# Kernel optimization log

Measured on AMD Instinct MI355X. Metric: run time of the kernel, lower is better.

Reference implementation:

```python
import jax, jax.numpy as jnp
import numpy as np

B, N, DIN = 8, 50000, 16
E, M, CH = 800000, 25000, 64
C_HALF = CH // 2


def setup_inputs() -> dict:
    key = jax.random.key(0)
    ks = jax.random.split(key, 9)
    x = jax.random.normal(ks[0], (B, N, DIN), dtype=jnp.float32)
    adj_rows = jax.random.randint(ks[1], (E,), 0, N, dtype=jnp.int32)
    adj_cols = jax.random.randint(ks[2], (E,), 0, N, dtype=jnp.int32)
    adj_vals = jax.random.uniform(ks[3], (E,), dtype=jnp.float32)
    centroids = jax.random.randint(ks[4], (M,), 0, N, dtype=jnp.int32)
    # Conv1d(kernel_size=1) weights == dense [out, in] matrices
    W_lin = jax.random.normal(ks[5], (C_HALF, DIN), dtype=jnp.float32) * (1.0 / np.sqrt(DIN))
    b_lin = jax.random.normal(ks[6], (C_HALF,), dtype=jnp.float32) * 0.01
    W_eye = jax.random.normal(ks[7], (C_HALF, DIN), dtype=jnp.float32) * (1.0 / np.sqrt(DIN))
    b_eye = jax.random.normal(ks[8], (C_HALF,), dtype=jnp.float32) * 0.01
    return {"x": x, "adj_rows": adj_rows, "adj_cols": adj_cols, "adj_vals": adj_vals,
            "centroids": centroids, "W_lin": W_lin, "b_lin": b_lin,
            "W_eye": W_eye, "b_eye": b_eye}


def reference(x, adj_rows, adj_cols, adj_vals, centroids, W_lin, b_lin, W_eye, b_eye):
    # x: [B, N, DIN] -> permute to channels-first [B, DIN, N]
    xc = jnp.transpose(x, (0, 2, 1))
    # eye branch: 1x1 conv == pointwise linear over channel dim
    eye_x = jnp.einsum('bcn,oc->bon', xc, W_eye) + b_eye[None, :, None]  # [B, C/2, N]
    # SpMM aggregation: adj @ x.T where x is [B*DIN, N]
    xt = xc.reshape(-1, xc.shape[-1]).T                      # [N, B*DIN]
    msgs = adj_vals[:, None] * xt[adj_cols]                  # [E, B*DIN] gather
    agg = jax.ops.segment_sum(msgs, adj_rows, num_segments=xt.shape[0])  # [N, B*DIN] scatter-add
    xa = agg.T.reshape(xc.shape)                             # [B, DIN, N]
    lin_x = jnp.einsum('bcn,oc->bon', xa, W_lin) + b_lin[None, :, None]  # [B, C/2, N]
    out = jax.nn.relu(jnp.concatenate([lin_x, eye_x], axis=1))  # [B, C, N]
    out = out[:, :, centroids]                               # gather centroid nodes [B, C, M]
    return jnp.transpose(out, (0, 2, 1))                     # [B, M, C]
```

## Files before the change

kernel.cpp:

```cpp
#include <hip/hip_runtime.h>

#define DIN   16
#define BB    8
#define FDIM  128
#define CHALF 32
#define CH    64
#define CAP   52
#define CAP2  16

__device__ __forceinline__ unsigned bf16rne(float f) {
    unsigned u = __float_as_uint(f);
    return (u + 0x7FFFu + ((u >> 16) & 1u)) >> 16;
}

__global__ __launch_bounds__(256) void prep_kernel(
    const float4* __restrict__ x4, uint2* __restrict__ xt2, int N,
    const int* __restrict__ centroids, int* __restrict__ seen,
    int* __restrict__ rankid, int* __restrict__ active_list,
    int* __restrict__ nactive, int* __restrict__ cnt2, int* __restrict__ mlist,
    int M) {
    int y = blockIdx.y;
    int t = blockIdx.x * 256 + threadIdx.x;
    if (y < BB) {
        if (t >= N * 4) return;
        int n = t >> 2;
        int q = t & 3;
        float4 v = x4[(long long)y * N * 4 + t];
        uint2 o;
        o.x = bf16rne(v.x) | (bf16rne(v.y) << 16);
        o.y = bf16rne(v.z) | (bf16rne(v.w) << 16);
        xt2[(long long)n * 32 + y * 4 + q] = o;
    } else {
        if (t >= M) return;
        int n = centroids[t];
        if (atomicExch(&seen[n], 1) == 0) {
            int r = atomicAdd(nactive, 1);
            rankid[n] = r + 1;
            active_list[r] = n;
        }
        int pos = atomicAdd(&cnt2[n], 1);
        if (pos < CAP2) mlist[n * CAP2 + pos] = t;
    }
}

__global__ __launch_bounds__(256) void bin_kernel(
    const int* __restrict__ rows, const int* __restrict__ cols,
    const float* __restrict__ vals, const int* __restrict__ rankid,
    int* __restrict__ cnt, int2* __restrict__ bins, int E) {
    int idx = blockIdx.x * blockDim.x + threadIdx.x;
    int e0 = idx * 2;
    if (e0 >= E) return;
    int2   r2 = ((const int2*)rows)[idx];
    int2   c2 = ((const int2*)cols)[idx];
    float2 v2 = ((const float2*)vals)[idx];
    int rr0 = rankid[r2.x];
    if (rr0 != 0) {
        int a = rr0 - 1;
        int pos = atomicAdd(&cnt[a], 1);
        if (pos < CAP)
            bins[(long long)a * CAP + pos] = make_int2(c2.x, __float_as_int(v2.x));
    }
    if (e0 + 1 < E) {
        int rr1 = rankid[r2.y];
        if (rr1 != 0) {
            int a = rr1 - 1;
            int pos = atomicAdd(&cnt[a], 1);
            if (pos < CAP)
                bins[(long long)a * CAP + pos] = make_int2(c2.y, __float_as_int(v2.y));
        }
    }
}

__global__ __launch_bounds__(256) void gather_kernel(
    const uint2* __restrict__ xt2, const int* __restrict__ cnt,
    const int2* __restrict__ bins, const int* __restrict__ active_list,
    const int* __restrict__ nactive,
    const int* __restrict__ cnt2, const int* __restrict__ mlist,
    const float* __restrict__ W_lin, const float* __restrict__ b_lin,
    const float* __restrict__ W_eye, const float* __restrict__ b_eye,
    float* __restrict__ out, int M) {
    int tid = threadIdx.x;
    int w = tid >> 6;
    int l = tid & 63;

    __shared__ float sWc[DIN][CH + 1];
    __shared__ float sb[CH];
    __shared__ float sagg[4][FDIM];
    __shared__ float sx[4][FDIM];

    #pragma unroll
    for (int i = tid; i < CH * DIN; i += 256) {
        int o = i >> 4, cc = i & 15;
        sWc[cc][o] = (o < CHALF) ? W_lin[i] : W_eye[i - CHALF * DIN];
    }
    if (tid < CHALF) sb[tid] = b_lin[tid];
    else if (tid < CH) sb[tid] = b_eye[tid - CHALF];
    __syncthreads();

    int a = blockIdx.x * 4 + w;
    if (a >= *nactive) return;
    int n = active_list[a];
    int c = min(cnt[a], CAP);

    int g = l >> 5;
    int s = l & 31;

    int2 myedge = make_int2(0, 0);
    if (l < c) myedge = bins[(long long)a * CAP + l];
    uint2 xraw = make_uint2(0u, 0u);
    if (g == 0) xraw = xt2[(long long)n * 32 + s];

    int iters = (c + 3) >> 2;
    float4 acc = make_float4(0.f, 0.f, 0.f, 0.f);
    for (int i = 0; i < iters; ++i) {
        int k0 = 4 * i + g;
        int k1 = k0 + 2;
        int   col0 = __shfl(myedge.x, k0);
        float v0   = __int_as_float(__shfl(myedge.y, k0));
        int   col1 = __shfl(myedge.x, k1);
        float v1   = __int_as_float(__shfl(myedge.y, k1));
        uint2 u0 = xt2[(long long)col0 * 32 + s];
        uint2 u1 = xt2[(long long)col1 * 32 + s];
        acc.x += v0 * __uint_as_float(u0.x << 16);
        acc.y += v0 * __uint_as_float(u0.x & 0xFFFF0000u);
        acc.z += v0 * __uint_as_float(u0.y << 16);
        acc.w += v0 * __uint_as_float(u0.y & 0xFFFF0000u);
        acc.x += v1 * __uint_as_float(u1.x << 16);
        acc.y += v1 * __uint_as_float(u1.x & 0xFFFF0000u);
        acc.z += v1 * __uint_as_float(u1.y << 16);
        acc.w += v1 * __uint_as_float(u1.y & 0xFFFF0000u);
    }
    acc.x += __shfl_xor(acc.x, 32);
    acc.y += __shfl_xor(acc.y, 32);
    acc.z += __shfl_xor(acc.z, 32);
    acc.w += __shfl_xor(acc.w, 32);
    if (g == 0) {
        ((float4*)sagg[w])[s] = acc;
        float4 xr;
        xr.x = __uint_as_float(xraw.x << 16);
        xr.y = __uint_as_float(xraw.x & 0xFFFF0000u);
        xr.z = __uint_as_float(xraw.y << 16);
        xr.w = __uint_as_float(xraw.y & 0xFFFF0000u);
        ((float4*)sx[w])[s] = xr;
    }

    int o = l;
    float wreg[DIN];
    #pragma unroll
    for (int cc = 0; cc < DIN; ++cc) wreg[cc] = sWc[cc][o];
    const float* src = (o < CHALF) ? sagg[w] : sx[w];
    float bias = sb[o];
    float res[BB];
    #pragma unroll
    for (int b = 0; b < BB; ++b) {
        float r = bias;
        #pragma unroll
        for (int cc = 0; cc < DIN; ++cc) r += wreg[cc] * src[b * DIN + cc];
        res[b] = fmaxf(r, 0.f);
    }

    int nm = min(cnt2[n], CAP2);
    for (int mm = 0; mm < nm; ++mm) {
        int m = mlist[n * CAP2 + mm];
        float* dst = out + (long long)m * CH + o;
        #pragma unroll
        for (int b = 0; b < BB; ++b)
            dst[(long long)b * M * CH] = res[b];
    }
}

extern "C" void kernel_launch(void* const* d_in, const int* in_sizes, int n_in,
                              void* d_out, int out_size, void* d_ws, size_t ws_size,
                              hipStream_t stream) {
    const float* x        = (const float*)d_in[0];
    const int*   adj_rows = (const int*)d_in[1];
    const int*   adj_cols = (const int*)d_in[2];
    const float* adj_vals = (const float*)d_in[3];
    const int*   cents    = (const int*)d_in[4];
    const float* W_lin    = (const float*)d_in[5];
    const float* b_lin    = (const float*)d_in[6];
    const float* W_eye    = (const float*)d_in[7];
    const float* b_eye    = (const float*)d_in[8];
    float* out = (float*)d_out;

    const int E = in_sizes[1];
    const int M = in_sizes[4];
    const int N = in_sizes[0] / (BB * DIN);

    char* p = (char*)d_ws;
    uint2* xt2   = (uint2*)p;   p += (size_t)N * 32 * sizeof(uint2);
    int2*  bins  = (int2*)p;    p += (size_t)M * CAP * sizeof(int2);
    int*   mlist = (int*)p;     p += (size_t)N * CAP2 * sizeof(int);
    int*   alist = (int*)p;     p += (size_t)M * sizeof(int);
    char* zbase = p;
    int* seen    = (int*)p;     p += (size_t)N * sizeof(int);
    int* rankid  = (int*)p;     p += (size_t)N * sizeof(int);
    int* cnt     = (int*)p;     p += (size_t)M * sizeof(int);
    int* cnt2    = (int*)p;     p += (size_t)N * sizeof(int);
    int* nactive = (int*)p;     p += 16 * sizeof(int);
    size_t zbytes = (size_t)(p - zbase);

    hipMemsetAsync(zbase, 0, zbytes, stream);

    dim3 pgrid((N * 4 + 255) / 256, BB + 1);
    prep_kernel<<<pgrid, 256, 0, stream>>>((const float4*)x, xt2, N,
                                           cents, seen, rankid, alist, nactive,
                                           cnt2, mlist, M);

    bin_kernel<<<(E / 2 + 255) / 256, 256, 0, stream>>>(adj_rows, adj_cols, adj_vals,
                                                        rankid, cnt, bins, E);

    int gblocks = (M + 3) / 4;
    gather_kernel<<<gblocks, 256, 0, stream>>>(xt2, cnt, bins, alist, nactive,
                                               cnt2, mlist,
                                               W_lin, b_lin, W_eye, b_eye, out, M);
}
```

Before: 159.4 us.

## Fuse memset, prep, bin and gather into one cooperative persistent kernel

Replaces the memset and three separate kernel launches with a single cooperative kernel. A bounded grid of persistent blocks uses grid-stride loops and separates the zeroing, transpose/centroid-marking, edge binning and gather/linear phases with grid.sync(). The intent is to remove launch overheads and inter-kernel gaps. In exchange, every phase is limited to the capped grid, which trims parallelism in the gather phase, and each grid-wide barrier has its own cost.

```diff
diff --git a/kernel.cpp b/kernel.cpp
--- a/kernel.cpp
+++ b/kernel.cpp
@@ -1,4 +1,7 @@
 #include <hip/hip_runtime.h>
+#include <hip/hip_cooperative_groups.h>
+
+namespace cg = cooperative_groups;
 
 #define DIN   16
 #define BB    8
@@ -7,31 +10,57 @@
 #define CH    64
 #define CAP   52
 #define CAP2  16
+#define NCU   256
 
 __device__ __forceinline__ unsigned bf16rne(float f) {
     unsigned u = __float_as_uint(f);
     return (u + 0x7FFFu + ((u >> 16) & 1u)) >> 16;
 }
 
-__global__ __launch_bounds__(256) void prep_kernel(
+__global__ __launch_bounds__(256, 4) void fused_kernel(
     const float4* __restrict__ x4, uint2* __restrict__ xt2, int N,
-    const int* __restrict__ centroids, int* __restrict__ seen,
-    int* __restrict__ rankid, int* __restrict__ active_list,
-    int* __restrict__ nactive, int* __restrict__ cnt2, int* __restrict__ mlist,
-    int M) {
-    int y = blockIdx.y;
-    int t = blockIdx.x * 256 + threadIdx.x;
-    if (y < BB) {
-        if (t >= N * 4) return;
-        int n = t >> 2;
-        int q = t & 3;
-        float4 v = x4[(long long)y * N * 4 + t];
+    const int* __restrict__ centroids, int* __restrict__ zbase, int zwords,
+    int* __restrict__ seen, int* __restrict__ rankid,
+    int* __restrict__ active_list, int* __restrict__ nactive,
+    int* __restrict__ cnt2, int* __restrict__ mlist, int M,
+    const int* __restrict__ rows, const int* __restrict__ cols,
+    const float* __restrict__ vals, int* __restrict__ cnt,
+    int2* __restrict__ bins, int E,
+    const float* __restrict__ W_lin, const float* __restrict__ b_lin,
+    const float* __restrict__ W_eye, const float* __restrict__ b_eye,
+    float* __restrict__ out)
+{
+    cg::grid_group grid = cg::this_grid();
+    const int tid   = threadIdx.x;
+    const int gtid  = blockIdx.x * 256 + tid;
+    const int gsize = gridDim.x * 256;
+
+    __shared__ float sWc[DIN][CH + 1];
+    __shared__ float sb[CH];
+    __shared__ float sagg[4][FDIM];
+    __shared__ float sx[4][FDIM];
+
+    for (int i = tid; i < CH * DIN; i += 256) {
+        int o = i >> 4, cc = i & 15;
+        sWc[cc][o] = (o < CHALF) ? W_lin[i] : W_eye[i - CHALF * DIN];
+    }
+    if (tid < CHALF) sb[tid] = b_lin[tid];
+    else if (tid < CH) sb[tid] = b_eye[tid - CHALF];
+
+    for (int i = gtid; i < zwords; i += gsize) zbase[i] = 0;
+
+    grid.sync();
+
+    const int TW = N * 32;
+    for (int i = gtid; i < TW; i += gsize) {
+        int n = i >> 5, slot = i & 31, b = slot >> 2, q = slot & 3;
+        float4 v = x4[((long long)b * N + n) * 4 + q];
         uint2 o;
         o.x = bf16rne(v.x) | (bf16rne(v.y) << 16);
         o.y = bf16rne(v.z) | (bf16rne(v.w) << 16);
-        xt2[(long long)n * 32 + y * 4 + q] = o;
-    } else {
-        if (t >= M) return;
+        xt2[i] = o;
+    }
+    for (int t = gtid; t < M; t += gsize) {
         int n = centroids[t];
         if (atomicExch(&seen[n], 1) == 0) {
             int r = atomicAdd(nactive, 1);
@@ -41,26 +70,21 @@
         int pos = atomicAdd(&cnt2[n], 1);
         if (pos < CAP2) mlist[n * CAP2 + pos] = t;
     }
-}
-
-__global__ __launch_bounds__(256) void bin_kernel(
-    const int* __restrict__ rows, const int* __restrict__ cols,
-    const float* __restrict__ vals, const int* __restrict__ rankid,
-    int* __restrict__ cnt, int2* __restrict__ bins, int E) {
-    int idx = blockIdx.x * blockDim.x + threadIdx.x;
-    int e0 = idx * 2;
-    if (e0 >= E) return;
-    int2   r2 = ((const int2*)rows)[idx];
-    int2   c2 = ((const int2*)cols)[idx];
-    float2 v2 = ((const float2*)vals)[idx];
-    int rr0 = rankid[r2.x];
-    if (rr0 != 0) {
-        int a = rr0 - 1;
-        int pos = atomicAdd(&cnt[a], 1);
-        if (pos < CAP)
-            bins[(long long)a * CAP + pos] = make_int2(c2.x, __float_as_int(v2.x));
-    }
-    if (e0 + 1 < E) {
+
+    grid.sync();
+
+    const int EP = E >> 1;
+    for (int idx = gtid; idx < EP; idx += gsize) {
+        int2   r2 = ((const int2*)rows)[idx];
+        int2   c2 = ((const int2*)cols)[idx];
+        float2 v2 = ((const float2*)vals)[idx];
+        int rr0 = rankid[r2.x];
+        if (rr0 != 0) {
+            int a = rr0 - 1;
+            int pos = atomicAdd(&cnt[a], 1);
+            if (pos < CAP)
+                bins[(long long)a * CAP + pos] = make_int2(c2.x, __float_as_int(v2.x));
+        }
         int rr1 = rankid[r2.y];
         if (rr1 != 0) {
             int a = rr1 - 1;
@@ -69,110 +93,90 @@
                 bins[(long long)a * CAP + pos] = make_int2(c2.y, __float_as_int(v2.y));
         }
     }
-}
-
-__global__ __launch_bounds__(256) void gather_kernel(
-    const uint2* __restrict__ xt2, const int* __restrict__ cnt,
-    const int2* __restrict__ bins, const int* __restrict__ active_list,
-    const int* __restrict__ nactive,
-    const int* __restrict__ cnt2, const int* __restrict__ mlist,
-    const float* __restrict__ W_lin, const float* __restrict__ b_lin,
-    const float* __restrict__ W_eye, const float* __restrict__ b_eye,
-    float* __restrict__ out, int M) {
-    int tid = threadIdx.x;
-    int w = tid >> 6;
-    int l = tid & 63;
-
-    __shared__ float sWc[DIN][CH + 1];
-    __shared__ float sb[CH];
-    __shared__ float sagg[4][FDIM];
-    __shared__ float sx[4][FDIM];
-
-    #pragma unroll
-    for (int i = tid; i < CH * DIN; i += 256) {
-        int o = i >> 4, cc = i & 15;
-        sWc[cc][o] = (o < CHALF) ? W_lin[i] : W_eye[i - CHALF * DIN];
-    }
-    if (tid < CHALF) sb[tid] = b_lin[tid];
-    else if (tid < CH) sb[tid] = b_eye[tid - CHALF];
-    __syncthreads();
-
-    int a = blockIdx.x * 4 + w;
-    if (a >= *nactive) return;
-    int n = active_list[a];
-    int c = min(cnt[a], CAP);
-
-    int g = l >> 5;
-    int s = l & 31;
-
-    int2 myedge = make_int2(0, 0);
-    if (l < c) myedge = bins[(long long)a * CAP + l];
-    uint2 xraw = make_uint2(0u, 0u);
-    if (g == 0) xraw = xt2[(long long)n * 32 + s];
-
-    int iters = (c + 3) >> 2;
-    float4 acc = make_float4(0.f, 0.f, 0.f, 0.f);
-    for (int i = 0; i < iters; ++i) {
-        int k0 = 4 * i + g;
-        int k1 = k0 + 2;
-        int   col0 = __shfl(myedge.x, k0);
-        float v0   = __int_as_float(__shfl(myedge.y, k0));
-        int   col1 = __shfl(myedge.x, k1);
-        float v1   = __int_as_float(__shfl(myedge.y, k1));
-        uint2 u0 = xt2[(long long)col0 * 32 + s];
-        uint2 u1 = xt2[(long long)col1 * 32 + s];
-        acc.x += v0 * __uint_as_float(u0.x << 16);
-        acc.y += v0 * __uint_as_float(u0.x & 0xFFFF0000u);
-        acc.z += v0 * __uint_as_float(u0.y << 16);
-        acc.w += v0 * __uint_as_float(u0.y & 0xFFFF0000u);
-        acc.x += v1 * __uint_as_float(u1.x << 16);
-        acc.y += v1 * __uint_as_float(u1.x & 0xFFFF0000u);
-        acc.z += v1 * __uint_as_float(u1.y << 16);
-        acc.w += v1 * __uint_as_float(u1.y & 0xFFFF0000u);
-    }
-    acc.x += __shfl_xor(acc.x, 32);
-    acc.y += __shfl_xor(acc.y, 32);
-    acc.z += __shfl_xor(acc.z, 32);
-    acc.w += __shfl_xor(acc.w, 32);
-    if (g == 0) {
-        ((float4*)sagg[w])[s] = acc;
-        float4 xr;
-        xr.x = __uint_as_float(xraw.x << 16);
-        xr.y = __uint_as_float(xraw.x & 0xFFFF0000u);
-        xr.z = __uint_as_float(xraw.y << 16);
-        xr.w = __uint_as_float(xraw.y & 0xFFFF0000u);
-        ((float4*)sx[w])[s] = xr;
-    }
-
-    int o = l;
+
+    grid.sync();
+
+    const int w = tid >> 6;
+    const int l = tid & 63;
+    const int g = l >> 5;
+    const int s = l & 31;
+    const int nact = *nactive;
+    const int wgid = blockIdx.x * 4 + w;
+    const int nwaves = gridDim.x * 4;
+
     float wreg[DIN];
     #pragma unroll
-    for (int cc = 0; cc < DIN; ++cc) wreg[cc] = sWc[cc][o];
-    const float* src = (o < CHALF) ? sagg[w] : sx[w];
-    float bias = sb[o];
-    float res[BB];
-    #pragma unroll
-    for (int b = 0; b < BB; ++b) {
-        float r = bias;
+    for (int cc = 0; cc < DIN; ++cc) wreg[cc] = sWc[cc][l];
+    const float bias = sb[l];
+    const float* src = (l < CHALF) ? sagg[w] : sx[w];
+
+    for (int a = wgid; a < nact; a += nwaves) {
+        int n = active_list[a];
+        int c = min(cnt[a], CAP);
+
+        int2 myedge = make_int2(0, 0);
+        if (l < c) myedge = bins[(long long)a * CAP + l];
+        uint2 xraw = make_uint2(0u, 0u);
+        if (g == 0) xraw = xt2[(long long)n * 32 + s];
+
+        int iters = (c + 3) >> 2;
+        float4 acc = make_float4(0.f, 0.f, 0.f, 0.f);
+        for (int i = 0; i < iters; ++i) {
+            int k0 = 4 * i + g;
+            int k1 = k0 + 2;
+            int   col0 = __shfl(myedge.x, k0);
+            float v0   = __int_as_float(__shfl(myedge.y, k0));
+            int   col1 = __shfl(myedge.x, k1);
+            float v1   = __int_as_float(__shfl(myedge.y, k1));
+            uint2 u0 = xt2[(long long)col0 * 32 + s];
+            uint2 u1 = xt2[(long long)col1 * 32 + s];
+            acc.x += v0 * __uint_as_float(u0.x << 16);
+            acc.y += v0 * __uint_as_float(u0.x & 0xFFFF0000u);
+            acc.z += v0 * __uint_as_float(u0.y << 16);
+            acc.w += v0 * __uint_as_float(u0.y & 0xFFFF0000u);
+            acc.x += v1 * __uint_as_float(u1.x << 16);
+            acc.y += v1 * __uint_as_float(u1.x & 0xFFFF0000u);
+            acc.z += v1 * __uint_as_float(u1.y << 16);
+            acc.w += v1 * __uint_as_float(u1.y & 0xFFFF0000u);
+        }
+        acc.x += __shfl_xor(acc.x, 32);
+        acc.y += __shfl_xor(acc.y, 32);
+        acc.z += __shfl_xor(acc.z, 32);
+        acc.w += __shfl_xor(acc.w, 32);
+        if (g == 0) {
+            ((float4*)sagg[w])[s] = acc;
+            float4 xr;
+            xr.x = __uint_as_float(xraw.x << 16);
+            xr.y = __uint_as_float(xraw.x & 0xFFFF0000u);
+            xr.z = __uint_as_float(xraw.y << 16);
+            xr.w = __uint_as_float(xraw.y & 0xFFFF0000u);
+            ((float4*)sx[w])[s] = xr;
+        }
+
+        float res[BB];
         #pragma unroll
-        for (int cc = 0; cc < DIN; ++cc) r += wreg[cc] * src[b * DIN + cc];
-        res[b] = fmaxf(r, 0.f);
-    }
-
-    int nm = min(cnt2[n], CAP2);
-    for (int mm = 0; mm < nm; ++mm) {
-        int m = mlist[n * CAP2 + mm];
-        float* dst = out + (long long)m * CH + o;
-        #pragma unroll
-        for (int b = 0; b < BB; ++b)
-            dst[(long long)b * M * CH] = res[b];
+        for (int b = 0; b < BB; ++b) {
+            float r = bias;
+            #pragma unroll
+            for (int cc = 0; cc < DIN; ++cc) r += wreg[cc] * src[b * DIN + cc];
+            res[b] = fmaxf(r, 0.f);
+        }
+
+        int nm = min(cnt2[n], CAP2);
+        for (int mm = 0; mm < nm; ++mm) {
+            int m = mlist[n * CAP2 + mm];
+            float* dst = out + (long long)m * CH + l;
+            #pragma unroll
+            for (int b = 0; b < BB; ++b)
+                dst[(long long)b * M * CH] = res[b];
+        }
     }
 }
 
 extern "C" void kernel_launch(void* const* d_in, const int* in_sizes, int n_in,
                               void* d_out, int out_size, void* d_ws, size_t ws_size,
                               hipStream_t stream) {
-    const float* x        = (const float*)d_in[0];
+    const float4* x4    = (const float4*)d_in[0];
     const int*   adj_rows = (const int*)d_in[1];
     const int*   adj_cols = (const int*)d_in[2];
     const float* adj_vals = (const float*)d_in[3];
@@ -183,35 +187,43 @@
     const float* b_eye    = (const float*)d_in[8];
     float* out = (float*)d_out;
 
-    const int E = in_sizes[1];
-    const int M = in_sizes[4];
-    const int N = in_sizes[0] / (BB * DIN);
+    int E = in_sizes[1];
+    int M = in_sizes[4];
+    int N = in_sizes[0] / (BB * DIN);
 
     char* p = (char*)d_ws;
     uint2* xt2   = (uint2*)p;   p += (size_t)N * 32 * sizeof(uint2);
     int2*  bins  = (int2*)p;    p += (size_t)M * CAP * sizeof(int2);
     int*   mlist = (int*)p;     p += (size_t)N * CAP2 * sizeof(int);
     int*   alist = (int*)p;     p += (size_t)M * sizeof(int);
-    char* zbase = p;
+    int* zbase = (int*)p;
     int* seen    = (int*)p;     p += (size_t)N * sizeof(int);
     int* rankid  = (int*)p;     p += (size_t)N * sizeof(int);
     int* cnt     = (int*)p;     p += (size_t)M * sizeof(int);
     int* cnt2    = (int*)p;     p += (size_t)N * sizeof(int);
     int* nactive = (int*)p;     p += 16 * sizeof(int);
-    size_t zbytes = (size_t)(p - zbase);
-
-    hipMemsetAsync(zbase, 0, zbytes, stream);
-
-    dim3 pgrid((N * 4 + 255) / 256, BB + 1);
-    prep_kernel<<<pgrid, 256, 0, stream>>>((const float4*)x, xt2, N,
-                                           cents, seen, rankid, alist, nactive,
-                                           cnt2, mlist, M);
-
-    bin_kernel<<<(E / 2 + 255) / 256, 256, 0, stream>>>(adj_rows, adj_cols, adj_vals,
-                                                        rankid, cnt, bins, E);
-
-    int gblocks = (M + 3) / 4;
-    gather_kernel<<<gblocks, 256, 0, stream>>>(xt2, cnt, bins, alist, nactive,
-                                               cnt2, mlist,
-                                               W_lin, b_lin, W_eye, b_eye, out, M);
+    int zwords = 3 * N + M + 16;
+
+    static int gblocks = 0;
+    if (gblocks == 0) {
+        int maxb = 0;
+        if (hipOccupancyMaxActiveBlocksPerMultiprocessor(&maxb, fused_kernel, 256, 0)
+                != hipSuccess || maxb < 1)
+            maxb = 2;
+        long long total = (long long)maxb * NCU;
+        gblocks = (int)(total < 1024 ? total : 1024);
+    }
+
+    void* args[] = {
+        (void*)&x4, (void*)&xt2, (void*)&N,
+        (void*)&cents, (void*)&zbase, (void*)&zwords,
+        (void*)&seen, (void*)&rankid, (void*)&alist, (void*)&nactive,
+        (void*)&cnt2, (void*)&mlist, (void*)&M,
+        (void*)&adj_rows, (void*)&adj_cols, (void*)&adj_vals,
+        (void*)&cnt, (void*)&bins, (void*)&E,
+        (void*)&W_lin, (void*)&b_lin, (void*)&W_eye, (void*)&b_eye,
+        (void*)&out
+    };
+    hipLaunchCooperativeKernel(fused_kernel, dim3(gblocks), dim3(256),
+                               args, 0, stream);
 }
```

Measured after the change: 458.9 us. +188.0%, slower.
